# Performance work log

Hardware: AMD Instinct MI355X
Metric: run time of the kernel (lower is better)

## Reference

```python
import jax, jax.numpy as jnp
import numpy as np

N_NODES = 100000
N_EDGES = 3200000
IN_FEAT = 512
HID = 32
N_CLASSES = 10


def gcn_conv(x, W, b, src, dst, num_nodes):
    """PyG GCNConv: linear transform, then symmetric-normalized aggregation
    with self-loops. out_i = sum_{j->i} norm_ij * (x_j W) + d_i^{-1} * (x_i W) + b."""
    h = x @ W  # [N, out]
    ones = jnp.ones(src.shape[0], dtype=x.dtype)
    deg = jax.ops.segment_sum(ones, dst, num_segments=num_nodes) + 1.0  # +1 self-loop
    dinv = jax.lax.rsqrt(deg)
    norm = dinv[src] * dinv[dst]  # [E]
    msg = h[src] * norm[:, None]  # [E, out]
    agg = jax.ops.segment_sum(msg, dst, num_segments=num_nodes)
    agg = agg + h * (dinv * dinv)[:, None]  # self-loop term (norm = d^-1)
    return agg + b


def setup_inputs() -> dict:
    key = jax.random.key(0)
    ks = jax.random.split(key, 12)
    x0 = jax.random.normal(ks[0], (N_NODES, IN_FEAT), dtype=jnp.float32)
    edge_index = jax.random.randint(ks[1], (2, N_EDGES), 0, N_NODES, dtype=jnp.int64)
    batch = jnp.zeros((N_NODES,), dtype=jnp.int64)

    def glorot(k, shape):
        fan_in, fan_out = shape
        lim = jnp.sqrt(6.0 / (fan_in + fan_out)).astype(jnp.float32)
        return jax.random.uniform(k, shape, jnp.float32, -lim, lim)

    return {
        "x0": x0,
        "edge_index": edge_index,
        "batch": batch,
        "W1": glorot(ks[2], (IN_FEAT, HID)),
        "b1": jnp.zeros((HID,), jnp.float32),
        "W2": glorot(ks[3], (HID, HID)),
        "b2": jnp.zeros((HID,), jnp.float32),
        "W3": glorot(ks[4], (HID, HID)),
        "b3": jnp.zeros((HID,), jnp.float32),
        "lin1_W": glorot(ks[5], (HID, 16)),
        "lin1_b": jnp.zeros((16,), jnp.float32),
        "lin2_W": glorot(ks[6], (16, N_CLASSES)),
        "lin2_b": jnp.zeros((N_CLASSES,), jnp.float32),
    }


def reference(x0, edge_index, batch, W1, b1, W2, b2, W3, b3,
              lin1_W, lin1_b, lin2_W, lin2_b):
    src, dst = edge_index[0], edge_index[1]
    n = x0.shape[0]
    x1 = jax.nn.relu(gcn_conv(x0, W1, b1, src, dst, n))
    x2 = jax.nn.relu(gcn_conv(x1, W2, b2, src, dst, n))
    x3 = jax.nn.relu(gcn_conv(x2, W3, b3, src, dst, n))
    # NOTE: original code computes cat([x1,x2,x3]) but then uses only x3; we match that.
    x = jax.nn.relu(x3 @ lin1_W + lin1_b)
    # dropout p=0.5 is identity in eval mode
    x = x @ lin2_W + lin2_b
    return x
```

## Files before the change

kernel.cpp:

```cpp
#include <hip/hip_runtime.h>
#include <hip/hip_bf16.h>

typedef float f32x4 __attribute__((ext_vector_type(4)));

#define N_NODES 100000
#define NBUK 391
#define BSHIFT 8
#define HBLK 256

__global__ void k_detect(const int* __restrict__ ei, int* __restrict__ mode) {
    __shared__ int flag;
    if (threadIdx.x == 0) flag = 0;
    __syncthreads();
    int f = 0;
    for (int i = threadIdx.x; i < 4096; i += 256)
        if (ei[2 * i + 1] != 0) f = 1;
    if (f) flag = 1;
    __syncthreads();
    if (threadIdx.x == 0) *mode = flag;
}

__global__ __launch_bounds__(256) void k_hist(const int* __restrict__ ei,
                                              const int* __restrict__ mode,
                                              int* __restrict__ gh, int E, int chunk) {
    __shared__ int hist[NBUK];
    int tid = threadIdx.x, k = blockIdx.x;
    for (int b = tid; b < NBUK; b += 256) hist[b] = 0;
    __syncthreads();
    int m = *mode;
    int e0 = k * chunk, e1 = min(E, e0 + chunk);
    for (int e = e0 + tid; e < e1; e += 256) {
        int d = m ? ei[E + e] : ei[2 * (E + e)];
        if ((unsigned)d >= N_NODES) d = 0;
        atomicAdd(&hist[d >> BSHIFT], 1);
    }
    __syncthreads();
    for (int b = tid; b < NBUK; b += 256) gh[k * NBUK + b] = hist[b];
}

__global__ __launch_bounds__(256) void k_btot(const int* __restrict__ gh, int* __restrict__ btot) {
    __shared__ int s[256];
    int b = blockIdx.x, tid = threadIdx.x;
    s[tid] = gh[tid * NBUK + b];
    __syncthreads();
    for (int d = 128; d > 0; d >>= 1) {
        if (tid < d) s[tid] += s[tid + d];
        __syncthreads();
    }
    if (tid == 0) btot[b] = s[0];
}

__global__ void k_scan_btot(const int* __restrict__ btot, int* __restrict__ bbase,
                            int* __restrict__ rowptr, int E) {
    __shared__ int s[512];
    int tid = threadIdx.x;
    int v = (tid < NBUK) ? btot[tid] : 0;
    s[tid] = v;
    __syncthreads();
    for (int d = 1; d < 512; d <<= 1) {
        int t = (tid >= d) ? s[tid - d] : 0;
        __syncthreads();
        s[tid] += t;
        __syncthreads();
    }
    if (tid < NBUK) bbase[tid] = s[tid] - v;
    if (tid == 0) { bbase[NBUK] = E; rowptr[N_NODES] = E; }
}

__global__ __launch_bounds__(256) void k_scan_cols(int* __restrict__ gh, const int* __restrict__ bbase) {
    __shared__ int s[256];
    int b = blockIdx.x, tid = threadIdx.x;
    int v = gh[tid * NBUK + b];
    s[tid] = v;
    __syncthreads();
    for (int d = 1; d < 256; d <<= 1) {
        int t = (tid >= d) ? s[tid - d] : 0;
        __syncthreads();
        s[tid] += t;
        __syncthreads();
    }
    gh[tid * NBUK + b] = bbase[b] + s[tid] - v;
}

__global__ __launch_bounds__(256) void k_bucketize(const int* __restrict__ ei,
                                                   const int* __restrict__ mode,
                                                   const int* __restrict__ offs,
                                                   int2* __restrict__ bp, int E, int chunk) {
    __shared__ int cur[NBUK];
    int tid = threadIdx.x, k = blockIdx.x;
    for (int b = tid; b < NBUK; b += 256) cur[b] = offs[k * NBUK + b];
    __syncthreads();
    int m = *mode;
    int e0 = k * chunk, e1 = min(E, e0 + chunk);
    for (int e = e0 + tid; e < e1; e += 256) {
        int s, d;
        if (m) { s = ei[e]; d = ei[E + e]; }
        else   { s = ei[2 * e]; d = ei[2 * (E + e)]; }
        if ((unsigned)s >= N_NODES) s = 0;
        if ((unsigned)d >= N_NODES) d = 0;
        int pos = atomicAdd(&cur[d >> BSHIFT], 1);
        int2 p; p.x = s; p.y = d;
        bp[pos] = p;
    }
}

__global__ __launch_bounds__(256) void k_build_csr(const int2* __restrict__ bp,
                                                   const int* __restrict__ bbase,
                                                   int* __restrict__ rowptr,
                                                   float* __restrict__ dinv,
                                                   int* __restrict__ csr) {
    __shared__ int cnt[256];
    __shared__ int s[256];
    __shared__ int cur[256];
    int b = blockIdx.x, tid = threadIdx.x;
    int nb = b << BSHIFT;
    int estart = bbase[b], eend = bbase[b + 1];
    cnt[tid] = 0;
    __syncthreads();
    for (int e = estart + tid; e < eend; e += 256) {
        int2 p = bp[e];
        atomicAdd(&cnt[p.y - nb], 1);
    }
    __syncthreads();
    int v = cnt[tid];
    s[tid] = v;
    __syncthreads();
    for (int d = 1; d < 256; d <<= 1) {
        int t = (tid >= d) ? s[tid - d] : 0;
        __syncthreads();
        s[tid] += t;
        __syncthreads();
    }
    int excl = s[tid] - v;
    int node = nb + tid;
    if (node < N_NODES) {
        rowptr[node] = estart + excl;
        dinv[node] = rsqrtf((float)v + 1.0f);
    }
    cur[tid] = estart + excl;
    __syncthreads();
    for (int e = estart + tid; e < eend; e += 256) {
        int2 p = bp[e];
        int pos = atomicAdd(&cur[p.y - nb], 1);
        csr[pos] = p.x;
    }
}

__global__ __launch_bounds__(256) void k_gemm1(const float* __restrict__ X,
                                               const float* __restrict__ W,
                                               const float* __restrict__ dinv,
                                               float* __restrict__ H) {
    __shared__ float lds[8448];
    float* xs  = lds;
    float* wsw = lds + 4160;
    int tid = threadIdx.x;
    int row = tid & 63;
    int kc  = tid >> 6;
    long row0 = (long)blockIdx.x * 64;

    float acc[32];
#pragma unroll
    for (int c = 0; c < 32; c++) acc[c] = 0.f;

    for (int k0 = 0; k0 < 512; k0 += 64) {
        __syncthreads();
#pragma unroll
        for (int u = 0; u < 8; u++) {
            int idx = u * 256 + tid;
            wsw[idx] = W[k0 * 32 + idx];
        }
#pragma unroll
        for (int u = 0; u < 4; u++) {
            int idx = u * 256 + tid;
            int rr = idx >> 4, j = idx & 15;
            long grow = row0 + rr;
            f32x4 v = {0.f, 0.f, 0.f, 0.f};
            if (grow < N_NODES) v = *(const f32x4*)&X[grow * 512 + k0 + 4 * j];
            float* dp = &xs[rr * 65 + 4 * j];
            dp[0] = v.x; dp[1] = v.y; dp[2] = v.z; dp[3] = v.w;
        }
        __syncthreads();
        int kbase = kc * 16;
#pragma unroll
        for (int kk = 0; kk < 16; kk++) {
            float xk = xs[row * 65 + kbase + kk];
            const float* wrow = &wsw[(kbase + kk) * 32];
#pragma unroll
            for (int c = 0; c < 32; c += 4) {
                f32x4 wv = *(const f32x4*)&wrow[c];
                acc[c]     += xk * wv.x;
                acc[c + 1] += xk * wv.y;
                acc[c + 2] += xk * wv.z;
                acc[c + 3] += xk * wv.w;
            }
        }
    }
    __syncthreads();
#pragma unroll
    for (int c = 0; c < 32; c++) lds[(kc * 64 + row) * 33 + c] = acc[c];
    __syncthreads();
#pragma unroll
    for (int i = 0; i < 8; i++) {
        int o = i * 256 + tid;
        int r = o >> 5, c = o & 31;
        float sv = lds[r * 33 + c] + lds[(64 + r) * 33 + c]
                 + lds[(128 + r) * 33 + c] + lds[(192 + r) * 33 + c];
        long grow = row0 + r;
        if (grow < N_NODES) H[grow * 32 + c] = sv * dinv[grow];
    }
}

__device__ __forceinline__ float gather_sum(const float* __restrict__ Hf,
                                            const int* __restrict__ csr,
                                            int e0, int e1, int f) {
    float a0 = 0.f, a1 = 0.f, a2 = 0.f, a3 = 0.f;
    for (int base = e0; base < e1; base += 32) {
        int idx = base + f;
        int sl = (idx < e1) ? csr[idx] : 0;
        int mm = e1 - base;
        if (mm >= 32) {
#pragma unroll
            for (int j = 0; j < 32; j += 4) {
                int s0 = __shfl(sl, j, 32);
                int s1 = __shfl(sl, j + 1, 32);
                int s2 = __shfl(sl, j + 2, 32);
                int s3 = __shfl(sl, j + 3, 32);
                a0 += Hf[(long)s0 * 32];
                a1 += Hf[(long)s1 * 32];
                a2 += Hf[(long)s2 * 32];
                a3 += Hf[(long)s3 * 32];
            }
        } else {
            for (int j = 0; j < mm; j++) {
                int s0 = __shfl(sl, j, 32);
                a0 += Hf[(long)s0 * 32];
            }
        }
    }
    return (a0 + a1) + (a2 + a3);
}

__global__ __launch_bounds__(256) void k_agg_mm(const float* __restrict__ H,
                                                const int* __restrict__ rowptr,
                                                const int* __restrict__ csr,
                                                const float* __restrict__ dinv,
                                                const float* __restrict__ bias,
                                                const float* __restrict__ W,
                                                float* __restrict__ Hout, int n) {
    __shared__ float ws[1024];
    int tid = threadIdx.x;
    for (int t = tid; t < 1024; t += 256) ws[t] = W[t];
    __syncthreads();
    int node = blockIdx.x * 8 + (tid >> 5);
    int f = tid & 31;
    if (node >= n) return;
    int e0 = rowptr[node], e1 = rowptr[node + 1];
    const float* Hf = H + f;
    float asum = gather_sum(Hf, csr, e0, e1, f);
    float dv = dinv[node];
    float v = dv * (asum + Hf[(long)node * 32]) + bias[f];
    v = fmaxf(v, 0.f);
    float o = 0.f;
#pragma unroll
    for (int k = 0; k < 32; k++) {
        float vk = __shfl(v, k, 32);
        o += vk * ws[k * 32 + f];
    }
    Hout[(long)node * 32 + f] = o * dv;
}

__global__ __launch_bounds__(256) void k_agg_head(const float* __restrict__ H,
                                                  const int* __restrict__ rowptr,
                                                  const int* __restrict__ csr,
                                                  const float* __restrict__ dinv,
                                                  const float* __restrict__ bias,
                                                  const float* __restrict__ L1W,
                                                  const float* __restrict__ L1B,
                                                  const float* __restrict__ L2W,
                                                  const float* __restrict__ L2B,
                                                  float* __restrict__ out, int n) {
    __shared__ float w1[512];
    __shared__ float w2[160];
    __shared__ float bb1[16];
    __shared__ float bb2[10];
    int tid = threadIdx.x;
    for (int t = tid; t < 512; t += 256) w1[t] = L1W[t];
    if (tid < 160) w2[tid] = L2W[tid];
    if (tid < 16) bb1[tid] = L1B[tid];
    if (tid < 10) bb2[tid] = L2B[tid];
    __syncthreads();
    int node = blockIdx.x * 8 + (tid >> 5);
    int f = tid & 31;
    if (node >= n) return;
    int e0 = rowptr[node], e1 = rowptr[node + 1];
    const float* Hf = H + f;
    float asum = gather_sum(Hf, csr, e0, e1, f);
    float dv = dinv[node];
    float v = dv * (asum + Hf[(long)node * 32]) + bias[f];
    v = fmaxf(v, 0.f);
    int c1 = f & 15;
    float t1 = 0.f;
#pragma unroll
    for (int k = 0; k < 32; k++) {
        float vk = __shfl(v, k, 32);
        t1 += vk * w1[k * 16 + c1];
    }
    t1 = fmaxf(t1 + bb1[c1], 0.f);
    int c2 = (f < 10) ? f : 0;
    float o = 0.f;
#pragma unroll
    for (int k = 0; k < 16; k++) {
        float tk = __shfl(t1, k, 32);
        o += tk * w2[k * 10 + c2];
    }
    o += bb2[c2];
    if (f < 10) out[(long)node * 10 + f] = o;
}

extern "C" void kernel_launch(void* const* d_in, const int* in_sizes, int n_in,
                              void* d_out, int out_size, void* d_ws, size_t ws_size,
                              hipStream_t stream) {
    const float* x0 = (const float*)d_in[0];
    const int* ei = (const int*)d_in[1];
    const float* W1 = (const float*)d_in[3];
    const float* b1 = (const float*)d_in[4];
    const float* W2 = (const float*)d_in[5];
    const float* b2 = (const float*)d_in[6];
    const float* W3 = (const float*)d_in[7];
    const float* b3 = (const float*)d_in[8];
    const float* l1W = (const float*)d_in[9];
    const float* l1b = (const float*)d_in[10];
    const float* l2W = (const float*)d_in[11];
    const float* l2b = (const float*)d_in[12];

    const int E = in_sizes[1] / 2;
    const int N = N_NODES;

    char* w = (char*)d_ws;
    float* h      = (float*)(w);
    float* xb     = (float*)(w + 12800000);
    int2*  bp     = (int2*) (w);
    int*   gh     = (int*)  (w + 25600000);
    int*   btot   = (int*)  (w + 26000384);
    int*   bbase  = (int*)  (w + 26001948);
    int*   rowptr = (int*)  (w + 26003516);
    float* dinv   = (float*)(w + 26403532);
    int*   csr    = (int*)  (w + 26803532);
    int*   mode   = (int*)  (w + 39603532);

    const int chunk = (E + HBLK - 1) / HBLK;
    const int AGB = (N + 7) / 8;
    const int G1B = (N + 63) / 64;

    k_detect<<<1, 256, 0, stream>>>(ei, mode);
    k_hist<<<HBLK, 256, 0, stream>>>(ei, mode, gh, E, chunk);
    k_btot<<<NBUK, 256, 0, stream>>>(gh, btot);
    k_scan_btot<<<1, 512, 0, stream>>>(btot, bbase, rowptr, E);
    k_scan_cols<<<NBUK, 256, 0, stream>>>(gh, bbase);
    k_bucketize<<<HBLK, 256, 0, stream>>>(ei, mode, gh, bp, E, chunk);
    k_build_csr<<<NBUK, 256, 0, stream>>>(bp, bbase, rowptr, dinv, csr);

    k_gemm1<<<G1B, 256, 0, stream>>>(x0, W1, dinv, h);
    k_agg_mm<<<AGB, 256, 0, stream>>>(h, rowptr, csr, dinv, b1, W2, xb, N);
    k_agg_mm<<<AGB, 256, 0, stream>>>(xb, rowptr, csr, dinv, b2, W3, h, N);
    k_agg_head<<<AGB, 256, 0, stream>>>(h, rowptr, csr, dinv, b3,
                                        l1W, l1b, l2W, l2b, (float*)d_out, N);
}
```

Baseline: 792.7 us.

## Store node features in fp16 and split aggregation into feature-half passes

Intermediate node features H and X are stored as half2 instead of float, halving the bytes moved by the random neighbor gathers. Aggregation is split into two passes over feature halves of 16 columns each, which shrinks the gathered working set per pass so it fits better in cache. The dense 32x32 transforms and the MLP head move into separate per-row kernels. The first GEMM is restructured to one row per thread, reading W straight from global memory instead of LDS. This adds fp16 rounding error and more kernel launches.

```diff
diff --git a/kernel.cpp b/kernel.cpp
--- a/kernel.cpp
+++ b/kernel.cpp
@@ -1,5 +1,5 @@
 #include <hip/hip_runtime.h>
-#include <hip/hip_bf16.h>
+#include <hip/hip_fp16.h>
 
 typedef float f32x4 __attribute__((ext_vector_type(4)));
 
@@ -146,18 +146,13 @@
     }
 }
 
-__global__ __launch_bounds__(256) void k_gemm1(const float* __restrict__ X,
+__global__ __launch_bounds__(128) void k_gemm1(const float* __restrict__ X,
                                                const float* __restrict__ W,
                                                const float* __restrict__ dinv,
-                                               float* __restrict__ H) {
-    __shared__ float lds[8448];
-    float* xs  = lds;
-    float* wsw = lds + 4160;
+                                               __half2* __restrict__ H2) {
+    __shared__ float xs[128 * 65];
     int tid = threadIdx.x;
-    int row = tid & 63;
-    int kc  = tid >> 6;
-    long row0 = (long)blockIdx.x * 64;
-
+    long row0 = (long)blockIdx.x * 128;
     float acc[32];
 #pragma unroll
     for (int c = 0; c < 32; c++) acc[c] = 0.f;
@@ -165,29 +160,24 @@
     for (int k0 = 0; k0 < 512; k0 += 64) {
         __syncthreads();
 #pragma unroll
-        for (int u = 0; u < 8; u++) {
-            int idx = u * 256 + tid;
-            wsw[idx] = W[k0 * 32 + idx];
-        }
-#pragma unroll
-        for (int u = 0; u < 4; u++) {
-            int idx = u * 256 + tid;
-            int rr = idx >> 4, j = idx & 15;
-            long grow = row0 + rr;
+        for (int u = 0; u < 16; u++) {
+            int idx = u * 128 + tid;
+            int r = idx >> 4, j = idx & 15;
+            long grow = row0 + r;
             f32x4 v = {0.f, 0.f, 0.f, 0.f};
             if (grow < N_NODES) v = *(const f32x4*)&X[grow * 512 + k0 + 4 * j];
-            float* dp = &xs[rr * 65 + 4 * j];
+            float* dp = &xs[r * 65 + 4 * j];
             dp[0] = v.x; dp[1] = v.y; dp[2] = v.z; dp[3] = v.w;
         }
         __syncthreads();
-        int kbase = kc * 16;
-#pragma unroll
-        for (int kk = 0; kk < 16; kk++) {
-            float xk = xs[row * 65 + kbase + kk];
-            const float* wrow = &wsw[(kbase + kk) * 32];
+        const float* xr = &xs[tid * 65];
+#pragma unroll
+        for (int kk = 0; kk < 64; kk++) {
+            float xk = xr[kk];
+            const float* wr = &W[(long)(k0 + kk) * 32];
 #pragma unroll
             for (int c = 0; c < 32; c += 4) {
-                f32x4 wv = *(const f32x4*)&wrow[c];
+                f32x4 wv = *(const f32x4*)&wr[c];
                 acc[c]     += xk * wv.x;
                 acc[c + 1] += xk * wv.y;
                 acc[c + 2] += xk * wv.z;
@@ -195,126 +185,128 @@
             }
         }
     }
-    __syncthreads();
-#pragma unroll
-    for (int c = 0; c < 32; c++) lds[(kc * 64 + row) * 33 + c] = acc[c];
-    __syncthreads();
-#pragma unroll
-    for (int i = 0; i < 8; i++) {
-        int o = i * 256 + tid;
-        int r = o >> 5, c = o & 31;
-        float sv = lds[r * 33 + c] + lds[(64 + r) * 33 + c]
-                 + lds[(128 + r) * 33 + c] + lds[(192 + r) * 33 + c];
-        long grow = row0 + r;
-        if (grow < N_NODES) H[grow * 32 + c] = sv * dinv[grow];
-    }
-}
-
-__device__ __forceinline__ float gather_sum(const float* __restrict__ Hf,
-                                            const int* __restrict__ csr,
-                                            int e0, int e1, int f) {
-    float a0 = 0.f, a1 = 0.f, a2 = 0.f, a3 = 0.f;
-    for (int base = e0; base < e1; base += 32) {
-        int idx = base + f;
+    long row = row0 + tid;
+    if (row < N_NODES) {
+        float dv = dinv[row];
+        __half2* hp = &H2[row * 16];
+#pragma unroll
+        for (int c = 0; c < 16; c++)
+            hp[c] = __floats2half2_rn(acc[2 * c] * dv, acc[2 * c + 1] * dv);
+    }
+}
+
+__global__ __launch_bounds__(256) void k_agg(const __half2* __restrict__ H2,
+                                             const int* __restrict__ rowptr,
+                                             const int* __restrict__ csr,
+                                             const float* __restrict__ dinv,
+                                             const float* __restrict__ bias,
+                                             __half2* __restrict__ X2, int po) {
+    int tid = threadIdx.x;
+    int node = blockIdx.x * 32 + (tid >> 3);
+    int l = tid & 7;
+    int off = po + l;
+    int e0 = rowptr[node], e1 = rowptr[node + 1];
+    float ax = 0.f, ay = 0.f;
+    for (int base = e0; base < e1; base += 8) {
+        int idx = base + l;
         int sl = (idx < e1) ? csr[idx] : 0;
-        int mm = e1 - base;
-        if (mm >= 32) {
-#pragma unroll
-            for (int j = 0; j < 32; j += 4) {
-                int s0 = __shfl(sl, j, 32);
-                int s1 = __shfl(sl, j + 1, 32);
-                int s2 = __shfl(sl, j + 2, 32);
-                int s3 = __shfl(sl, j + 3, 32);
-                a0 += Hf[(long)s0 * 32];
-                a1 += Hf[(long)s1 * 32];
-                a2 += Hf[(long)s2 * 32];
-                a3 += Hf[(long)s3 * 32];
+        int cnt = e1 - base;
+        if (cnt >= 8) {
+#pragma unroll
+            for (int j = 0; j < 8; j++) {
+                int s = __shfl(sl, j, 8);
+                float2 v = __half22float2(H2[(long)s * 16 + off]);
+                ax += v.x; ay += v.y;
             }
         } else {
-            for (int j = 0; j < mm; j++) {
-                int s0 = __shfl(sl, j, 32);
-                a0 += Hf[(long)s0 * 32];
+            for (int j = 0; j < cnt; j++) {
+                int s = __shfl(sl, j, 8);
+                float2 v = __half22float2(H2[(long)s * 16 + off]);
+                ax += v.x; ay += v.y;
             }
         }
     }
-    return (a0 + a1) + (a2 + a3);
-}
-
-__global__ __launch_bounds__(256) void k_agg_mm(const float* __restrict__ H,
-                                                const int* __restrict__ rowptr,
-                                                const int* __restrict__ csr,
-                                                const float* __restrict__ dinv,
-                                                const float* __restrict__ bias,
-                                                const float* __restrict__ W,
-                                                float* __restrict__ Hout, int n) {
-    __shared__ float ws[1024];
-    int tid = threadIdx.x;
-    for (int t = tid; t < 1024; t += 256) ws[t] = W[t];
-    __syncthreads();
-    int node = blockIdx.x * 8 + (tid >> 5);
-    int f = tid & 31;
-    if (node >= n) return;
-    int e0 = rowptr[node], e1 = rowptr[node + 1];
-    const float* Hf = H + f;
-    float asum = gather_sum(Hf, csr, e0, e1, f);
     float dv = dinv[node];
-    float v = dv * (asum + Hf[(long)node * 32]) + bias[f];
-    v = fmaxf(v, 0.f);
-    float o = 0.f;
+    float2 sf = __half22float2(H2[(long)node * 16 + off]);
+    float2 bv = *(const float2*)&bias[2 * off];
+    float vx = fmaxf(dv * (ax + sf.x) + bv.x, 0.f);
+    float vy = fmaxf(dv * (ay + sf.y) + bv.y, 0.f);
+    X2[(long)node * 16 + off] = __floats2half2_rn(vx, vy);
+}
+
+__global__ __launch_bounds__(256) void k_mm(const __half2* __restrict__ X2,
+                                            const float* __restrict__ W,
+                                            const float* __restrict__ dinv,
+                                            __half2* __restrict__ H2, int n) {
+    int r = blockIdx.x * 256 + threadIdx.x;
+    if (r >= n) return;
+    float x[32];
+#pragma unroll
+    for (int i = 0; i < 16; i++) {
+        float2 v = __half22float2(X2[(long)r * 16 + i]);
+        x[2 * i] = v.x; x[2 * i + 1] = v.y;
+    }
+    float acc[32];
+#pragma unroll
+    for (int c = 0; c < 32; c++) acc[c] = 0.f;
 #pragma unroll
     for (int k = 0; k < 32; k++) {
-        float vk = __shfl(v, k, 32);
-        o += vk * ws[k * 32 + f];
-    }
-    Hout[(long)node * 32 + f] = o * dv;
-}
-
-__global__ __launch_bounds__(256) void k_agg_head(const float* __restrict__ H,
-                                                  const int* __restrict__ rowptr,
-                                                  const int* __restrict__ csr,
-                                                  const float* __restrict__ dinv,
-                                                  const float* __restrict__ bias,
-                                                  const float* __restrict__ L1W,
-                                                  const float* __restrict__ L1B,
-                                                  const float* __restrict__ L2W,
-                                                  const float* __restrict__ L2B,
-                                                  float* __restrict__ out, int n) {
-    __shared__ float w1[512];
-    __shared__ float w2[160];
-    __shared__ float bb1[16];
-    __shared__ float bb2[10];
-    int tid = threadIdx.x;
-    for (int t = tid; t < 512; t += 256) w1[t] = L1W[t];
-    if (tid < 160) w2[tid] = L2W[tid];
-    if (tid < 16) bb1[tid] = L1B[tid];
-    if (tid < 10) bb2[tid] = L2B[tid];
-    __syncthreads();
-    int node = blockIdx.x * 8 + (tid >> 5);
-    int f = tid & 31;
-    if (node >= n) return;
-    int e0 = rowptr[node], e1 = rowptr[node + 1];
-    const float* Hf = H + f;
-    float asum = gather_sum(Hf, csr, e0, e1, f);
-    float dv = dinv[node];
-    float v = dv * (asum + Hf[(long)node * 32]) + bias[f];
-    v = fmaxf(v, 0.f);
-    int c1 = f & 15;
-    float t1 = 0.f;
+        float xk = x[k];
+        const float* wr = &W[k * 32];
+#pragma unroll
+        for (int c = 0; c < 32; c += 4) {
+            f32x4 wv = *(const f32x4*)&wr[c];
+            acc[c]     += xk * wv.x;
+            acc[c + 1] += xk * wv.y;
+            acc[c + 2] += xk * wv.z;
+            acc[c + 3] += xk * wv.w;
+        }
+    }
+    float dv = dinv[r];
+    __half2* hp = &H2[(long)r * 16];
+#pragma unroll
+    for (int c = 0; c < 16; c++)
+        hp[c] = __floats2half2_rn(acc[2 * c] * dv, acc[2 * c + 1] * dv);
+}
+
+__global__ __launch_bounds__(256) void k_head(const __half2* __restrict__ X2,
+                                              const float* __restrict__ L1W,
+                                              const float* __restrict__ L1B,
+                                              const float* __restrict__ L2W,
+                                              const float* __restrict__ L2B,
+                                              float* __restrict__ out, int n) {
+    int r = blockIdx.x * 256 + threadIdx.x;
+    if (r >= n) return;
+    float x[32];
+#pragma unroll
+    for (int i = 0; i < 16; i++) {
+        float2 v = __half22float2(X2[(long)r * 16 + i]);
+        x[2 * i] = v.x; x[2 * i + 1] = v.y;
+    }
+    float t1[16];
+#pragma unroll
+    for (int c = 0; c < 16; c++) t1[c] = L1B[c];
 #pragma unroll
     for (int k = 0; k < 32; k++) {
-        float vk = __shfl(v, k, 32);
-        t1 += vk * w1[k * 16 + c1];
-    }
-    t1 = fmaxf(t1 + bb1[c1], 0.f);
-    int c2 = (f < 10) ? f : 0;
-    float o = 0.f;
+        float xk = x[k];
+        const float* wr = &L1W[k * 16];
+#pragma unroll
+        for (int c = 0; c < 16; c++) t1[c] += xk * wr[c];
+    }
+#pragma unroll
+    for (int c = 0; c < 16; c++) t1[c] = fmaxf(t1[c], 0.f);
+    float o[10];
+#pragma unroll
+    for (int c = 0; c < 10; c++) o[c] = L2B[c];
 #pragma unroll
     for (int k = 0; k < 16; k++) {
-        float tk = __shfl(t1, k, 32);
-        o += tk * w2[k * 10 + c2];
-    }
-    o += bb2[c2];
-    if (f < 10) out[(long)node * 10 + f] = o;
+        float tk = t1[k];
+        const float* wr = &L2W[k * 10];
+#pragma unroll
+        for (int c = 0; c < 10; c++) o[c] += tk * wr[c];
+    }
+#pragma unroll
+    for (int c = 0; c < 10; c++) out[(long)r * 10 + c] = o[c];
 }
 
 extern "C" void kernel_launch(void* const* d_in, const int* in_sizes, int n_in,
@@ -337,8 +329,8 @@
     const int N = N_NODES;
 
     char* w = (char*)d_ws;
-    float* h      = (float*)(w);
-    float* xb     = (float*)(w + 12800000);
+    __half2* h2   = (__half2*)(w);
+    __half2* x2   = (__half2*)(w + 6400000);
     int2*  bp     = (int2*) (w);
     int*   gh     = (int*)  (w + 25600000);
     int*   btot   = (int*)  (w + 26000384);
@@ -349,8 +341,9 @@
     int*   mode   = (int*)  (w + 39603532);
 
     const int chunk = (E + HBLK - 1) / HBLK;
-    const int AGB = (N + 7) / 8;
-    const int G1B = (N + 63) / 64;
+    const int AGB = (N + 31) / 32;
+    const int G1B = (N + 127) / 128;
+    const int NB  = (N + 255) / 256;
 
     k_detect<<<1, 256, 0, stream>>>(ei, mode);
     k_hist<<<HBLK, 256, 0, stream>>>(ei, mode, gh, E, chunk);
@@ -360,9 +353,14 @@
     k_bucketize<<<HBLK, 256, 0, stream>>>(ei, mode, gh, bp, E, chunk);
     k_build_csr<<<NBUK, 256, 0, stream>>>(bp, bbase, rowptr, dinv, csr);
 
-    k_gemm1<<<G1B, 256, 0, stream>>>(x0, W1, dinv, h);
-    k_agg_mm<<<AGB, 256, 0, stream>>>(h, rowptr, csr, dinv, b1, W2, xb, N);
-    k_agg_mm<<<AGB, 256, 0, stream>>>(xb, rowptr, csr, dinv, b2, W3, h, N);
-    k_agg_head<<<AGB, 256, 0, stream>>>(h, rowptr, csr, dinv, b3,
-                                        l1W, l1b, l2W, l2b, (float*)d_out, N);
-}
+    k_gemm1<<<G1B, 128, 0, stream>>>(x0, W1, dinv, h2);
+    k_agg<<<AGB, 256, 0, stream>>>(h2, rowptr, csr, dinv, b1, x2, 0);
+    k_agg<<<AGB, 256, 0, stream>>>(h2, rowptr, csr, dinv, b1, x2, 8);
+    k_mm<<<NB, 256, 0, stream>>>(x2, W2, dinv, h2, N);
+    k_agg<<<AGB, 256, 0, stream>>>(h2, rowptr, csr, dinv, b2, x2, 0);
+    k_agg<<<AGB, 256, 0, stream>>>(h2, rowptr, csr, dinv, b2, x2, 8);
+    k_mm<<<NB, 256, 0, stream>>>(x2, W3, dinv, h2, N);
+    k_agg<<<AGB, 256, 0, stream>>>(h2, rowptr, csr, dinv, b3, x2, 0);
+    k_agg<<<AGB, 256, 0, stream>>>(h2, rowptr, csr, dinv, b3, x2, 8);
+    k_head<<<NB, 256, 0, stream>>>(x2, l1W, l1b, l2W, l2b, (float*)d_out, N);
+}
```

Result: slower. 815.2 us (+2.8%).
